# Kernel optimization log

Hardware: AMD Instinct MI355X
Metric: run time of the kernel (lower is better)

Reference implementation:

```python
import jax, jax.numpy as jnp
import numpy as np

N, D, K = 16384, 768, 10000

def setup_inputs() -> dict:
    key = jax.random.key(0)
    k1, k2 = jax.random.split(key)
    x = jax.random.normal(k1, (N, D), dtype=jnp.float32)
    centroids = jax.random.normal(k2, (D, K), dtype=jnp.float32)
    return {"x": x, "centroids": centroids}

def reference(x, centroids):
    x_norm = jnp.sum(x * x, axis=1, keepdims=True)            # [N, 1]
    c_norm = jnp.sum(centroids * centroids, axis=0)[None, :]  # [1, K]
    dist = x_norm - 2.0 * jnp.matmul(x, centroids) + c_norm   # [N, K]
    return jnp.argmin(dist, axis=-1)                          # [N]
```

## Files before the change

### kernel.cpp

```cpp
#include <hip/hip_runtime.h>
#include <cfloat>

#define N_ROWS 16384
#define DDIM   768
#define KCOLS  10000
#define KPAD   10112

#define TRANSC_BLKS (KPAD / 32 * (DDIM / 32))
#define CONVX_BLKS  (N_ROWS * 96 / 256)
#define CNORM_BLKS  (KPAD / 64)

typedef __attribute__((ext_vector_type(4))) float f32x4;
typedef __attribute__((ext_vector_type(8))) short s16x8;
typedef unsigned long long u64;
typedef unsigned int u32;

__device__ __forceinline__ u32 fsort(float f) {
  u32 u = __float_as_uint(f);
  return (u & 0x80000000u) ? ~u : (u | 0x80000000u);
}
__device__ __forceinline__ float funsort(u32 u) {
  u32 b = (u & 0x80000000u) ? (u ^ 0x80000000u) : ~u;
  return __uint_as_float(b);
}
__device__ __forceinline__ unsigned short f2bf(float f) {
  u32 b = __float_as_uint(f);
  return (unsigned short)((b + 0x7fffu + ((b >> 16) & 1u)) >> 16);
}
__device__ __forceinline__ float bf2f(unsigned short s) {
  return __uint_as_float(((u32)s) << 16);
}

__global__ __launch_bounds__(256) void prep_kernel(
    const float* __restrict__ X, const float* __restrict__ C,
    unsigned short* __restrict__ Xb, unsigned short* __restrict__ Cb,
    float* __restrict__ Ct, float* __restrict__ cn, u64* __restrict__ best) {
  __shared__ float smem[32 * 33];
  const int bid = blockIdx.x;
  const int t = threadIdx.x;

  if (bid < TRANSC_BLKS) {
    const int kk = (bid % (KPAD / 32)) * 32;
    const int dd = (bid / (KPAD / 32)) * 32;
    const int tx = t & 31, ty = t >> 5;
#pragma unroll
    for (int j = 0; j < 4; ++j) {
      int d = dd + ty + j * 8, k = kk + tx;
      smem[(ty + j * 8) * 33 + tx] = (k < KCOLS) ? C[(size_t)d * KCOLS + k] : 0.f;
    }
    __syncthreads();
#pragma unroll
    for (int j = 0; j < 4; ++j) {
      int k = kk + ty + j * 8, d = dd + tx;
      float v = smem[tx * 33 + (ty + j * 8)];
      Cb[(size_t)k * DDIM + (d ^ ((k & 7) << 3))] = f2bf(v);
      Ct[(size_t)k * DDIM + d] = v;
    }
  } else if (bid < TRANSC_BLKS + CONVX_BLKS) {
    int i = (bid - TRANSC_BLKS) * 256 + t;
    if (i < N_ROWS) best[i] = ~0ULL;
    int row = i / 96;
    int pc  = i % 96;
    int lc  = pc ^ (row & 7);
    const float4* p = (const float4*)(X + (size_t)row * DDIM + lc * 8);
    float4 a = p[0], b = p[1];
    union { unsigned short s[8]; uint4 v; } o;
    o.s[0] = f2bf(a.x); o.s[1] = f2bf(a.y); o.s[2] = f2bf(a.z); o.s[3] = f2bf(a.w);
    o.s[4] = f2bf(b.x); o.s[5] = f2bf(b.y); o.s[6] = f2bf(b.z); o.s[7] = f2bf(b.w);
    *((uint4*)Xb + i) = o.v;
  } else {
    const int kb = bid - TRANSC_BLKS - CONVX_BLKS;
    const int tx = t & 63, ty = t >> 6;
    const int k = kb * 64 + tx;
    float s = 0.f;
    if (k < KCOLS) {
      const float* p = C + (size_t)(ty * 192) * KCOLS + k;
      for (int d = 0; d < 192; ++d) {
        float v = p[(size_t)d * KCOLS];
        s = fmaf(v, v, s);
      }
    }
    smem[ty * 64 + tx] = s;
    __syncthreads();
    if (ty == 0)
      cn[k] = (k < KCOLS)
                  ? ((smem[tx] + smem[64 + tx]) + (smem[128 + tx] + smem[192 + tx]))
                  : FLT_MAX;
  }
}

#define GLOAD_LDS16(gp, lp)                                                     \
  __builtin_amdgcn_global_load_lds((const __attribute__((address_space(1))) void*)(gp), \
                                   (__attribute__((address_space(3))) void*)(lp), 16, 0, 0)

__global__ __launch_bounds__(256) void seed_mfma(
    const unsigned short* __restrict__ Xb, const unsigned short* __restrict__ Cb,
    const float* __restrict__ cn, u32* __restrict__ amin) {
  __shared__ unsigned short As[128 * 64];
  __shared__ unsigned short Bs[64 * 64];

  const int t = threadIdx.x;
  const int lane = t & 63, wave = t >> 6;
  const int n0 = blockIdx.x * 128;
  const int lr = lane & 15, lg = lane >> 4;
  const int srow = lane >> 3, schunk = lane & 7;
  const int xra = lr & 7;
  const int xrb = (lr * 6) & 7;

  f32x4 acc[2][4];
  f32x4 z = {0.f, 0.f, 0.f, 0.f};
#pragma unroll
  for (int m = 0; m < 2; ++m)
#pragma unroll
    for (int n = 0; n < 4; ++n) acc[m][n] = z;

  const unsigned short* gA = Xb + (size_t)(n0 + wave * 32 + srow) * DDIM + schunk * 8;
  const unsigned short* gB = Cb + (size_t)(wave * 16 + srow) * 158 * DDIM + schunk * 8;

  for (int it = 0; it < DDIM / 64; ++it) {
#pragma unroll
    for (int i = 0; i < 4; ++i)
      GLOAD_LDS16(gA + (size_t)i * 8 * DDIM, As + (wave * 32 + i * 8) * 64);
#pragma unroll
    for (int i = 0; i < 2; ++i)
      GLOAD_LDS16(gB + (size_t)i * 8 * 158 * DDIM, Bs + (wave * 16 + i * 8) * 64);
    gA += 64; gB += 64;
    __syncthreads();
#pragma unroll
    for (int dk = 0; dk < 2; ++dk) {
      s16x8 af[2], bfr[4];
#pragma unroll
      for (int m = 0; m < 2; ++m)
        af[m] = *(const s16x8*)(As + (wave * 32 + m * 16 + lr) * 64 + (((dk * 4 + lg) ^ xra) * 8));
#pragma unroll
      for (int n = 0; n < 4; ++n)
        bfr[n] = *(const s16x8*)(Bs + (n * 16 + lr) * 64 + (((dk * 4 + lg) ^ xrb) * 8));
#pragma unroll
      for (int m = 0; m < 2; ++m)
#pragma unroll
        for (int n = 0; n < 4; ++n)
          acc[m][n] = __builtin_amdgcn_mfma_f32_16x16x32_bf16(af[m], bfr[n], acc[m][n], 0, 0, 0);
    }
    __syncthreads();
  }

  float cnv[4];
#pragma unroll
  for (int n = 0; n < 4; ++n) cnv[n] = cn[(n * 16 + lr) * 158];

#pragma unroll
  for (int m = 0; m < 2; ++m) {
#pragma unroll
    for (int e = 0; e < 4; ++e) {
      float v = FLT_MAX;
#pragma unroll
      for (int n = 0; n < 4; ++n)
        v = fminf(v, fmaf(-2.f, acc[m][n][e], cnv[n]));
#pragma unroll
      for (int s = 1; s < 16; s <<= 1) v = fminf(v, __shfl_xor(v, s));
      if (lr == 0) amin[n0 + wave * 32 + m * 16 + lg * 4 + e] = fsort(v);
    }
  }
}


__global__ __launch_bounds__(256, 4) void assign_mfma(
    const unsigned short* __restrict__ Xb, const unsigned short* __restrict__ Cb,
    const float* __restrict__ X32, const float* __restrict__ C32,
    const float* __restrict__ Ct, const float* __restrict__ cn,
    u32* __restrict__ amin, u64* __restrict__ best) {
  __shared__ unsigned short As[128 * 64];
  __shared__ unsigned short Bs[128 * 64];

  const int t = threadIdx.x;
  const int lane = t & 63, wave = t >> 6;
  const int wr = wave >> 1, wc = wave & 1;
  const int n0 = blockIdx.x * 128;
  const int k0 = blockIdx.y * 128;
  const int lr = lane & 15, lg = lane >> 4;
  const int srow = lane >> 3, schunk = lane & 7;
  const int xr = lr & 7;

  f32x4 acc[4][4];
  f32x4 z = {0.f, 0.f, 0.f, 0.f};
#pragma unroll
  for (int m = 0; m < 4; ++m)
#pragma unroll
    for (int n = 0; n < 4; ++n) acc[m][n] = z;

  const unsigned short* gA = Xb + (size_t)(n0 + wave * 32 + srow) * DDIM + schunk * 8;
  const unsigned short* gB = Cb + (size_t)(k0 + wave * 32 + srow) * DDIM + schunk * 8;

  for (int it = 0; it < DDIM / 64; ++it) {
#pragma unroll
    for (int i = 0; i < 4; ++i) {
      GLOAD_LDS16(gA + (size_t)i * 8 * DDIM, As + (wave * 32 + i * 8) * 64);
      GLOAD_LDS16(gB + (size_t)i * 8 * DDIM, Bs + (wave * 32 + i * 8) * 64);
    }
    gA += 64; gB += 64;
    __syncthreads();
#pragma unroll
    for (int dk = 0; dk < 2; ++dk) {
      s16x8 af[4], bfr[4];
      const int c = (dk * 4 + lg) ^ xr;
#pragma unroll
      for (int m = 0; m < 4; ++m)
        af[m] = *(const s16x8*)(As + (wr * 64 + m * 16 + lr) * 64 + c * 8);
#pragma unroll
      for (int n = 0; n < 4; ++n)
        bfr[n] = *(const s16x8*)(Bs + (wc * 64 + n * 16 + lr) * 64 + c * 8);
#pragma unroll
      for (int m = 0; m < 4; ++m)
#pragma unroll
        for (int n = 0; n < 4; ++n)
          acc[m][n] = __builtin_amdgcn_mfma_f32_16x16x32_bf16(af[m], bfr[n], acc[m][n], 0, 0, 0);
    }
    __syncthreads();
  }

  float cnv[4];
#pragma unroll
  for (int n = 0; n < 4; ++n) cnv[n] = cn[k0 + wc * 64 + n * 16 + lr];

#pragma unroll
  for (int m = 0; m < 4; ++m) {
    float sc[4][4];
#pragma unroll
    for (int n = 0; n < 4; ++n)
#pragma unroll
      for (int e = 0; e < 4; ++e) sc[n][e] = fmaf(-2.f, acc[m][n][e], cnv[n]);

    float th[4];
#pragma unroll
    for (int e = 0; e < 4; ++e) {
      float v = fminf(fminf(sc[0][e], sc[1][e]), fminf(sc[2][e], sc[3][e]));
      u32 key = fsort(v);
#pragma unroll
      for (int s = 1; s < 16; s <<= 1) {
        u32 o = __shfl_xor(key, s);
        key = key < o ? key : o;
      }
      int row = n0 + wr * 64 + m * 16 + lg * 4 + e;
      u32 mr = key;
      if (lr == 0) {
        u32 old = atomicMin(&amin[row], key);
        mr = old < key ? old : key;
      }
      mr = __shfl(mr, lane & 48);
      th[e] = funsort(mr) + 1.5f;
    }

#pragma unroll
    for (int n = 0; n < 4; ++n) {
#pragma unroll
      for (int e = 0; e < 4; ++e) {
        int kq = k0 + wc * 64 + n * 16 + lr;
        bool cand = (kq < KCOLS) && (sc[n][e] <= th[e]);
        u64 mask = __ballot(cand);
        while (mask) {
          int src = (int)__builtin_ctzll(mask);
          mask &= mask - 1;
          int srowg = n0 + wr * 64 + m * 16 + ((src >> 4) & 3) * 4 + e;
          int skg = k0 + wc * 64 + n * 16 + (src & 15);
          float part = 0.f;
          const float* xp = X32 + (size_t)srowg * DDIM + lane;
          if (Ct) {
            const float* cp = Ct + (size_t)skg * DDIM + lane;
#pragma unroll
            for (int i = 0; i < 12; ++i)
              part = fmaf(xp[i * 64], cp[i * 64], part);
          } else {
            const float* cp = C32 + (size_t)lane * KCOLS + skg;
#pragma unroll
            for (int i = 0; i < 12; ++i)
              part = fmaf(xp[i * 64], cp[(size_t)i * 64 * KCOLS], part);
          }
#pragma unroll
          for (int s = 1; s < 64; s <<= 1) part += __shfl_xor(part, s);
          if (lane == 0) {
            float ex = fmaf(-2.f, part, cn[skg]);
            atomicMin(&best[srowg], ((u64)fsort(ex) << 32) | (u32)skg);
          }
        }
      }
    }
  }
}


__global__ void cnorm_kernel(const float* __restrict__ C, float* __restrict__ cnorm,
                             int D, int K) {
  int k = blockIdx.x * blockDim.x + threadIdx.x;
  if (k >= K) return;
  float s = 0.f;
  for (int d = 0; d < D; ++d) {
    float v = C[(size_t)d * K + k];
    s = fmaf(v, v, s);
  }
  cnorm[k] = s;
}

__global__ void init_kernel(u64* best, int N) {
  int n = blockIdx.x * blockDim.x + threadIdx.x;
  if (n < N) best[n] = ~0ULL;
}

__global__ __launch_bounds__(256) void assign_kernel(
    const float* __restrict__ X, const float* __restrict__ C,
    const float* __restrict__ cnorm, u64* __restrict__ best,
    int N, int D, int K) {
  __shared__ float Xs[16][128];
  __shared__ float Cs[16][64];
  const int t = threadIdx.x;
  const int tx = t & 15, ty = t >> 4;
  const int k0 = blockIdx.x * 64;
  const int n0 = blockIdx.y * 128;
  float acc[8][4];
#pragma unroll
  for (int i = 0; i < 8; ++i)
#pragma unroll
    for (int j = 0; j < 4; ++j) acc[i][j] = 0.f;
  for (int d0 = 0; d0 < D; d0 += 16) {
#pragma unroll
    for (int v = 0; v < 2; ++v) {
      int f4 = t + v * 256;
      int row = f4 >> 2;
      int dc = (f4 & 3) * 4;
      const float4 xv = *(const float4*)&X[(size_t)(n0 + row) * D + d0 + dc];
      Xs[dc + 0][row] = xv.x; Xs[dc + 1][row] = xv.y;
      Xs[dc + 2][row] = xv.z; Xs[dc + 3][row] = xv.w;
    }
    {
      int d = t >> 4, kc = (t & 15) * 4, k = k0 + kc;
      float4 cv;
      if (k + 3 < K) cv = *(const float4*)&C[(size_t)(d0 + d) * K + k];
      else {
        cv.x = (k + 0 < K) ? C[(size_t)(d0 + d) * K + k + 0] : 0.f;
        cv.y = (k + 1 < K) ? C[(size_t)(d0 + d) * K + k + 1] : 0.f;
        cv.z = (k + 2 < K) ? C[(size_t)(d0 + d) * K + k + 2] : 0.f;
        cv.w = (k + 3 < K) ? C[(size_t)(d0 + d) * K + k + 3] : 0.f;
      }
      *(float4*)&Cs[d][kc] = cv;
    }
    __syncthreads();
#pragma unroll
    for (int d = 0; d < 16; ++d) {
      float4 a0 = *(const float4*)&Xs[d][ty * 8];
      float4 a1 = *(const float4*)&Xs[d][ty * 8 + 4];
      float4 b = *(const float4*)&Cs[d][tx * 4];
      float av[8] = {a0.x, a0.y, a0.z, a0.w, a1.x, a1.y, a1.z, a1.w};
      float bv[4] = {b.x, b.y, b.z, b.w};
#pragma unroll
      for (int i = 0; i < 8; ++i)
#pragma unroll
        for (int j = 0; j < 4; ++j) acc[i][j] = fmaf(av[i], bv[j], acc[i][j]);
    }
    __syncthreads();
  }
  float cnv[4];
#pragma unroll
  for (int j = 0; j < 4; ++j) {
    int k = k0 + tx * 4 + j;
    cnv[j] = (k < K) ? cnorm[k] : 0.f;
  }
#pragma unroll
  for (int i = 0; i < 8; ++i) {
    u64 key = ~0ULL;
#pragma unroll
    for (int j = 0; j < 4; ++j) {
      int k = k0 + tx * 4 + j;
      if (k < K) {
        float score = fmaf(-2.f, acc[i][j], cnv[j]);
        u64 cand = ((u64)fsort(score) << 32) | (unsigned)k;
        key = key < cand ? key : cand;
      }
    }
#pragma unroll
    for (int mk = 8; mk >= 1; mk >>= 1) {
      u64 other = __shfl_xor(key, mk, 16);
      key = key < other ? key : other;
    }
    if (tx == 0) atomicMin(&best[n0 + ty * 8 + i], key);
  }
}

__global__ void out_kernel(const u64* __restrict__ best, int* __restrict__ out, int N) {
  int n = blockIdx.x * blockDim.x + threadIdx.x;
  if (n < N) out[n] = (int)(u32)(best[n] & 0xffffffffu);
}

extern "C" void kernel_launch(void* const* d_in, const int* in_sizes, int n_in,
                              void* d_out, int out_size, void* d_ws, size_t ws_size,
                              hipStream_t stream) {
  const float* X = (const float*)d_in[0];
  const float* C = (const float*)d_in[1];
  int* out = (int*)d_out;

  const size_t OFF_BEST = 0;
  const size_t OFF_AMIN = 131072;
  const size_t OFF_CN   = 196608;
  const size_t OFF_XB   = 262144;
  const size_t OFF_CB   = OFF_XB + (size_t)N_ROWS * DDIM * 2;
  const size_t OFF_CT   = OFF_CB + (size_t)KPAD * DDIM * 2;
  const size_t REQ_A    = OFF_CT + (size_t)KPAD * DDIM * 4;

  if (ws_size >= REQ_A) {
    u64* best = (u64*)((char*)d_ws + OFF_BEST);
    u32* amin = (u32*)((char*)d_ws + OFF_AMIN);
    float* cnp = (float*)((char*)d_ws + OFF_CN);
    unsigned short* Xb = (unsigned short*)((char*)d_ws + OFF_XB);
    unsigned short* Cb = (unsigned short*)((char*)d_ws + OFF_CB);
    float* Ct = (float*)((char*)d_ws + OFF_CT);

    hipLaunchKernelGGL(prep_kernel, dim3(TRANSC_BLKS + CONVX_BLKS + CNORM_BLKS), dim3(256),
                       0, stream, X, C, Xb, Cb, Ct, cnp, best);
    hipLaunchKernelGGL(seed_mfma, dim3(N_ROWS / 128), dim3(256), 0, stream, Xb, Cb, cnp, amin);
    hipLaunchKernelGGL(assign_mfma, dim3(N_ROWS / 128, KPAD / 128), dim3(256), 0, stream,
                       Xb, Cb, X, C, Ct, cnp, amin, best);
    hipLaunchKernelGGL(out_kernel, dim3(64), dim3(256), 0, stream, best, out, N_ROWS);
  } else {
    u64* best = (u64*)d_ws;
    float* cnorm = (float*)((char*)d_ws + (size_t)N_ROWS * sizeof(u64));
    hipLaunchKernelGGL(init_kernel, dim3(64), dim3(256), 0, stream, best, N_ROWS);
    hipLaunchKernelGGL(cnorm_kernel, dim3((KCOLS + 255) / 256), dim3(256), 0, stream,
                       C, cnorm, DDIM, KCOLS);
    hipLaunchKernelGGL(assign_kernel, dim3((KCOLS + 63) / 64, N_ROWS / 128), dim3(256), 0,
                       stream, X, C, cnorm, best, N_ROWS, DDIM, KCOLS);
    hipLaunchKernelGGL(out_kernel, dim3(64), dim3(256), 0, stream, best, out, N_ROWS);
  }
}
```

Measured before the change: 402.0 us.

## Rewrite assign GEMM as 256x256 8-wave double-buffered ping-pong pipeline

Replaces the 128x128, 4-wave, singly-buffered MFMA assign kernel with a 256x256 tile, 512-thread kernel. It double-buffers A and B in 128KB of LDS and interleaves global-to-LDS staging with MFMA quads, using explicit barriers, waitcnt and setprio. Blocks are remapped with an XCD-aware swizzle and K is padded to 10240. The aim is to hide load latency and raise operand reuse. The cost is one workgroup per CU, more padded work, and heavier per-block epilogues.

After: 600.1 us. +49.3%, slower.

```diff
diff --git a/kernel.cpp b/kernel.cpp
--- a/kernel.cpp
+++ b/kernel.cpp
@@ -4,7 +4,7 @@
 #define N_ROWS 16384
 #define DDIM   768
 #define KCOLS  10000
-#define KPAD   10112
+#define KPAD   10240
 
 #define TRANSC_BLKS (KPAD / 32 * (DDIM / 32))
 #define CONVX_BLKS  (N_ROWS * 96 / 256)
@@ -164,127 +164,169 @@
 }
 
 
-__global__ __launch_bounds__(256, 4) void assign_mfma(
+#define READ_A(AF, buf, mb) do {                                                  \
+  const unsigned short* _p = lds + (buf)*32768 + (wr*128 + (mb)*16 + lr)*64;      \
+  _Pragma("unroll") for (int dk = 0; dk < 2; ++dk)                                \
+  _Pragma("unroll") for (int m = 0; m < 4; ++m)                                   \
+    AF[dk][m] = *(const s16x8*)(_p + m*1024 + (((dk*4+lg)^xr)*8));                \
+} while (0)
+
+#define READ_B(BF, buf, nb) do {                                                  \
+  const unsigned short* _p = lds + (buf)*32768 + 16384 + (wc*64 + (nb)*16 + lr)*64;\
+  _Pragma("unroll") for (int dk = 0; dk < 2; ++dk)                                \
+  _Pragma("unroll") for (int n = 0; n < 2; ++n)                                   \
+    BF[dk][n] = *(const s16x8*)(_p + n*1024 + (((dk*4+lg)^xr)*8));                \
+} while (0)
+
+#define STAGE_A(buf, h, dch) do {                                                 \
+  GLOAD_LDS16(gAb + (size_t)((h)*128) * DDIM + (dch)*8,                           \
+              lds + (buf)*32768 + (h)*8192 + wave*512);                           \
+  GLOAD_LDS16(gAb + (size_t)((h)*128 + 64) * DDIM + (dch)*8,                      \
+              lds + (buf)*32768 + (h)*8192 + 4096 + wave*512);                    \
+} while (0)
+
+#define STAGE_B(buf, h, dch) do {                                                 \
+  GLOAD_LDS16(gBb + (size_t)((h)*128) * DDIM + (dch)*8,                           \
+              lds + 16384 + (buf)*32768 + (h)*8192 + wave*512);                   \
+  GLOAD_LDS16(gBb + (size_t)((h)*128 + 64) * DDIM + (dch)*8,                      \
+              lds + 16384 + (buf)*32768 + (h)*8192 + 4096 + wave*512);            \
+} while (0)
+
+#define PH_SYNC() do { __builtin_amdgcn_s_barrier();                              \
+  asm volatile("s_waitcnt lgkmcnt(0)" ::: "memory"); } while (0)
+#define PH_END() __builtin_amdgcn_s_barrier()
+#define CKPT() do { __builtin_amdgcn_sched_barrier(0);                            \
+  asm volatile("s_waitcnt vmcnt(4)" ::: "memory"); } while (0)
+
+#define QUAD(ACC, nb, BF) do {                                                    \
+  __builtin_amdgcn_s_setprio(1);                                                  \
+  _Pragma("unroll") for (int dk = 0; dk < 2; ++dk)                                \
+  _Pragma("unroll") for (int m = 0; m < 4; ++m)                                   \
+  _Pragma("unroll") for (int n = 0; n < 2; ++n)                                   \
+    ACC[m][(nb) + n] = __builtin_amdgcn_mfma_f32_16x16x32_bf16(                   \
+        af[dk][m], BF[dk][n], ACC[m][(nb) + n], 0, 0, 0);                         \
+  __builtin_amdgcn_s_setprio(0);                                                  \
+} while (0)
+
+#define EPILOG(ACC, MBASE) do {                                                   \
+  _Pragma("unroll") for (int m = 0; m < 4; ++m) {                                 \
+    float sc[4][4];                                                               \
+    _Pragma("unroll") for (int n = 0; n < 4; ++n)                                 \
+      _Pragma("unroll") for (int e = 0; e < 4; ++e)                               \
+        sc[n][e] = fmaf(-2.f, ACC[m][n][e], cnv[n]);                              \
+    float th[4];                                                                  \
+    _Pragma("unroll") for (int e = 0; e < 4; ++e) {                               \
+      float v = fminf(fminf(sc[0][e], sc[1][e]), fminf(sc[2][e], sc[3][e]));      \
+      u32 key = fsort(v);                                                         \
+      _Pragma("unroll") for (int s = 1; s < 16; s <<= 1) {                        \
+        u32 o = __shfl_xor(key, s);                                               \
+        key = key < o ? key : o;                                                  \
+      }                                                                           \
+      int row = n0 + wr * 128 + (MBASE) + m * 16 + lg * 4 + e;                    \
+      u32 mr = key;                                                               \
+      if (lr == 0) {                                                              \
+        u32 old = atomicMin(&amin[row], key);                                     \
+        mr = old < key ? old : key;                                               \
+      }                                                                           \
+      mr = __shfl(mr, lane & 48);                                                 \
+      th[e] = funsort(mr) + 1.5f;                                                 \
+    }                                                                             \
+    _Pragma("unroll") for (int n = 0; n < 4; ++n) {                               \
+      _Pragma("unroll") for (int e = 0; e < 4; ++e) {                             \
+        int kq = k0 + wc * 64 + n * 16 + lr;                                      \
+        bool cand = (kq < KCOLS) && (sc[n][e] <= th[e]);                          \
+        u64 mask = __ballot(cand);                                                \
+        while (mask) {                                                            \
+          int src = (int)__builtin_ctzll(mask);                                   \
+          mask &= mask - 1;                                                       \
+          int srowg = n0 + wr * 128 + (MBASE) + m * 16 + ((src >> 4) & 3) * 4 + e;\
+          int skg = k0 + wc * 64 + n * 16 + (src & 15);                           \
+          float part = 0.f;                                                       \
+          const float* xp = X32 + (size_t)srowg * DDIM + lane;                    \
+          const float* cp = Ct + (size_t)skg * DDIM + lane;                       \
+          _Pragma("unroll") for (int ii = 0; ii < 12; ++ii)                       \
+            part = fmaf(xp[ii * 64], cp[ii * 64], part);                          \
+          _Pragma("unroll") for (int s = 1; s < 64; s <<= 1)                      \
+            part += __shfl_xor(part, s);                                          \
+          if (lane == 0) {                                                        \
+            float ex = fmaf(-2.f, part, cn[skg]);                                 \
+            atomicMin(&best[srowg], ((u64)fsort(ex) << 32) | (u32)skg);           \
+          }                                                                       \
+        }                                                                         \
+      }                                                                           \
+    }                                                                             \
+  }                                                                               \
+} while (0)
+
+__global__ __launch_bounds__(512, 1) void assign_mfma8p(
     const unsigned short* __restrict__ Xb, const unsigned short* __restrict__ Cb,
-    const float* __restrict__ X32, const float* __restrict__ C32,
-    const float* __restrict__ Ct, const float* __restrict__ cn,
-    u32* __restrict__ amin, u64* __restrict__ best) {
-  __shared__ unsigned short As[128 * 64];
-  __shared__ unsigned short Bs[128 * 64];
+    const float* __restrict__ X32, const float* __restrict__ Ct,
+    const float* __restrict__ cn, u32* __restrict__ amin, u64* __restrict__ best) {
+  __shared__ __align__(16) unsigned short lds[65536];
 
   const int t = threadIdx.x;
   const int lane = t & 63, wave = t >> 6;
-  const int wr = wave >> 1, wc = wave & 1;
-  const int n0 = blockIdx.x * 128;
-  const int k0 = blockIdx.y * 128;
+  const int wr = wave >> 2, wc = wave & 3;
+  const int bid = blockIdx.x;
+  const int wg = (bid & 7) * 320 + (bid >> 3);
+  const int n0 = (wg / 40) * 256;
+  const int k0 = (wg % 40) * 256;
   const int lr = lane & 15, lg = lane >> 4;
-  const int srow = lane >> 3, schunk = lane & 7;
   const int xr = lr & 7;
 
-  f32x4 acc[4][4];
+  f32x4 accA[4][4], accB[4][4];
   f32x4 z = {0.f, 0.f, 0.f, 0.f};
 #pragma unroll
   for (int m = 0; m < 4; ++m)
 #pragma unroll
-    for (int n = 0; n < 4; ++n) acc[m][n] = z;
-
-  const unsigned short* gA = Xb + (size_t)(n0 + wave * 32 + srow) * DDIM + schunk * 8;
-  const unsigned short* gB = Cb + (size_t)(k0 + wave * 32 + srow) * DDIM + schunk * 8;
-
-  for (int it = 0; it < DDIM / 64; ++it) {
-#pragma unroll
-    for (int i = 0; i < 4; ++i) {
-      GLOAD_LDS16(gA + (size_t)i * 8 * DDIM, As + (wave * 32 + i * 8) * 64);
-      GLOAD_LDS16(gB + (size_t)i * 8 * DDIM, Bs + (wave * 32 + i * 8) * 64);
-    }
-    gA += 64; gB += 64;
-    __syncthreads();
-#pragma unroll
-    for (int dk = 0; dk < 2; ++dk) {
-      s16x8 af[4], bfr[4];
-      const int c = (dk * 4 + lg) ^ xr;
-#pragma unroll
-      for (int m = 0; m < 4; ++m)
-        af[m] = *(const s16x8*)(As + (wr * 64 + m * 16 + lr) * 64 + c * 8);
-#pragma unroll
-      for (int n = 0; n < 4; ++n)
-        bfr[n] = *(const s16x8*)(Bs + (wc * 64 + n * 16 + lr) * 64 + c * 8);
-#pragma unroll
-      for (int m = 0; m < 4; ++m)
-#pragma unroll
-        for (int n = 0; n < 4; ++n)
-          acc[m][n] = __builtin_amdgcn_mfma_f32_16x16x32_bf16(af[m], bfr[n], acc[m][n], 0, 0, 0);
-    }
-    __syncthreads();
+    for (int n = 0; n < 4; ++n) { accA[m][n] = z; accB[m][n] = z; }
+
+  const unsigned short* gAb = Xb + (size_t)(n0 + wave * 8 + (lane >> 3)) * DDIM + (lane & 7) * 8;
+  const unsigned short* gBb = Cb + (size_t)(k0 + wave * 8 + (lane >> 3)) * DDIM + (lane & 7) * 8;
+
+  s16x8 af[2][4], bf0[2][2], bf1[2][2];
+
+  STAGE_A(0, 0, 0); STAGE_A(0, 1, 0); STAGE_B(0, 0, 0); STAGE_B(0, 1, 0);
+  STAGE_B(1, 0, 8); STAGE_B(1, 1, 8);
+  CKPT();
+  __builtin_amdgcn_s_barrier();
+
+  for (int i = 0; i < 6; ++i) {
+    const int cA = (2 * i + 1) * 8;
+    const int c2 = ((2 * i + 2) % 12) * 8;
+    const int c3 = ((2 * i + 3) % 12) * 8;
+    READ_A(af, 0, 0); READ_B(bf0, 0, 0);
+    STAGE_A(1, 0, cA);
+    PH_SYNC(); QUAD(accA, 0, bf0); PH_END();
+    READ_B(bf1, 0, 2);
+    STAGE_A(1, 1, cA);
+    PH_SYNC(); QUAD(accA, 2, bf1); PH_END();
+    READ_A(af, 0, 4);
+    STAGE_B(0, 0, c2);
+    PH_SYNC(); QUAD(accB, 2, bf1); PH_END();
+    STAGE_B(0, 1, c2);
+    CKPT();
+    PH_SYNC(); QUAD(accB, 0, bf0); PH_END();
+    READ_A(af, 1, 0); READ_B(bf0, 1, 0);
+    STAGE_A(0, 0, c2);
+    PH_SYNC(); QUAD(accA, 0, bf0); PH_END();
+    READ_B(bf1, 1, 2);
+    STAGE_A(0, 1, c2);
+    PH_SYNC(); QUAD(accA, 2, bf1); PH_END();
+    READ_A(af, 1, 4);
+    STAGE_B(1, 0, c3);
+    PH_SYNC(); QUAD(accB, 2, bf1); PH_END();
+    STAGE_B(1, 1, c3);
+    CKPT();
+    PH_SYNC(); QUAD(accB, 0, bf0); PH_END();
   }
 
   float cnv[4];
 #pragma unroll
   for (int n = 0; n < 4; ++n) cnv[n] = cn[k0 + wc * 64 + n * 16 + lr];
 
-#pragma unroll
-  for (int m = 0; m < 4; ++m) {
-    float sc[4][4];
-#pragma unroll
-    for (int n = 0; n < 4; ++n)
-#pragma unroll
-      for (int e = 0; e < 4; ++e) sc[n][e] = fmaf(-2.f, acc[m][n][e], cnv[n]);
-
-    float th[4];
-#pragma unroll
-    for (int e = 0; e < 4; ++e) {
-      float v = fminf(fminf(sc[0][e], sc[1][e]), fminf(sc[2][e], sc[3][e]));
-      u32 key = fsort(v);
-#pragma unroll
-      for (int s = 1; s < 16; s <<= 1) {
-        u32 o = __shfl_xor(key, s);
-        key = key < o ? key : o;
-      }
-      int row = n0 + wr * 64 + m * 16 + lg * 4 + e;
-      u32 mr = key;
-      if (lr == 0) {
-        u32 old = atomicMin(&amin[row], key);
-        mr = old < key ? old : key;
-      }
-      mr = __shfl(mr, lane & 48);
-      th[e] = funsort(mr) + 1.5f;
-    }
-
-#pragma unroll
-    for (int n = 0; n < 4; ++n) {
-#pragma unroll
-      for (int e = 0; e < 4; ++e) {
-        int kq = k0 + wc * 64 + n * 16 + lr;
-        bool cand = (kq < KCOLS) && (sc[n][e] <= th[e]);
-        u64 mask = __ballot(cand);
-        while (mask) {
-          int src = (int)__builtin_ctzll(mask);
-          mask &= mask - 1;
-          int srowg = n0 + wr * 64 + m * 16 + ((src >> 4) & 3) * 4 + e;
-          int skg = k0 + wc * 64 + n * 16 + (src & 15);
-          float part = 0.f;
-          const float* xp = X32 + (size_t)srowg * DDIM + lane;
-          if (Ct) {
-            const float* cp = Ct + (size_t)skg * DDIM + lane;
-#pragma unroll
-            for (int i = 0; i < 12; ++i)
-              part = fmaf(xp[i * 64], cp[i * 64], part);
-          } else {
-            const float* cp = C32 + (size_t)lane * KCOLS + skg;
-#pragma unroll
-            for (int i = 0; i < 12; ++i)
-              part = fmaf(xp[i * 64], cp[(size_t)i * 64 * KCOLS], part);
-          }
-#pragma unroll
-          for (int s = 1; s < 64; s <<= 1) part += __shfl_xor(part, s);
-          if (lane == 0) {
-            float ex = fmaf(-2.f, part, cn[skg]);
-            atomicMin(&best[srowg], ((u64)fsort(ex) << 32) | (u32)skg);
-          }
-        }
-      }
-    }
-  }
+  EPILOG(accA, 0);
+  EPILOG(accB, 64);
 }
 
 
@@ -415,8 +457,8 @@
     hipLaunchKernelGGL(prep_kernel, dim3(TRANSC_BLKS + CONVX_BLKS + CNORM_BLKS), dim3(256),
                        0, stream, X, C, Xb, Cb, Ct, cnp, best);
     hipLaunchKernelGGL(seed_mfma, dim3(N_ROWS / 128), dim3(256), 0, stream, Xb, Cb, cnp, amin);
-    hipLaunchKernelGGL(assign_mfma, dim3(N_ROWS / 128, KPAD / 128), dim3(256), 0, stream,
-                       Xb, Cb, X, C, Ct, cnp, amin, best);
+    hipLaunchKernelGGL(assign_mfma8p, dim3((N_ROWS / 256) * (KPAD / 256)), dim3(512), 0, stream,
+                       Xb, Cb, X, Ct, cnp, amin, best);
     hipLaunchKernelGGL(out_kernel, dim3(64), dim3(256), 0, stream, best, out, N_ROWS);
   } else {
     u64* best = (u64*)d_ws;
```
